# Performance work log

Measured on AMD Instinct MI355X. Metric: run time of the kernel, lower is better.

Reference implementation:

```python
import jax, jax.numpy as jnp
import numpy as np
import math

H = 128      # hidden_size
B = 4        # bsz
N = 32       # bsz * num_doc_per_q
L = 128      # doc_len


def setup_inputs() -> dict:
    key = jax.random.key(0)
    ks = jax.random.split(key, 7)
    word_ent_info = jax.random.normal(ks[0], (N, L, H), dtype=jnp.float32)
    word_ent_info_mask = jax.random.randint(ks[1], (N, L), 0, 2, dtype=jnp.int32)
    doc = jax.random.normal(ks[2], (N, L, H), dtype=jnp.float32)
    doc_mask = jax.random.randint(ks[3], (N, L), 0, 2, dtype=jnp.int32)
    q_for_text = jax.random.normal(ks[4], (B, H), dtype=jnp.float32)
    # nn.Linear(3H, H): weight [H, 3H], bias [H]
    W1 = jax.random.normal(ks[5], (H, 3 * H), dtype=jnp.float32) / math.sqrt(3 * H)
    b1 = jnp.zeros((H,), dtype=jnp.float32)
    # nn.Linear(H, 1): weight [1, H], bias [1]
    w2 = jax.random.normal(ks[6], (1, H), dtype=jnp.float32) / math.sqrt(H)
    b2 = jnp.zeros((1,), dtype=jnp.float32)
    return {"word_ent_info": word_ent_info, "word_ent_info_mask": word_ent_info_mask,
            "doc": doc, "doc_mask": doc_mask, "q_for_text": q_for_text,
            "W1": W1, "b1": b1, "w2": w2, "b2": b2}


def reference(word_ent_info, word_ent_info_mask, doc, doc_mask, q_for_text, W1, b1, w2, b2):
    n, l, h = doc.shape
    bsz = q_for_text.shape[0]
    dt = doc.dtype

    # word_ent_infoagg = mask^T @ word_ent_info -> [N, H]
    m = word_ent_info_mask.astype(dt)
    ent_agg = jnp.einsum('nl,nlh->nh', m, word_ent_info)

    # q expanded to one row per document: [N, H]
    q_exp = jnp.repeat(q_for_text, n // bsz, axis=0)

    # Split W1 over the concat([doc_self, ent_agg, q_agg]) feature axis.
    # score_pre[n,j,k,:] = W1a @ (doc_j*doc_k) + W1b @ (doc_j*ent_agg) + W1c @ (doc_k*q)
    W1a, W1b, W1c = jnp.split(W1, 3, axis=1)        # each [H, H]
    A = jnp.einsum('nje,nke,ge->njkg', doc, doc, W1a)          # [N,L,L,H]
    Bt = jnp.einsum('nje,ge->njg', doc * ent_agg[:, None, :], W1b)  # [N,L,H]
    Ct = jnp.einsum('nke,ge->nkg', doc * q_exp[:, None, :], W1c)    # [N,L,H]
    hid = jnp.tanh(A + Bt[:, :, None, :] + Ct[:, None, :, :] + b1)  # [N,L,L,H]

    score = (jnp.einsum('njkg,g->njk', hid, w2[0]) + b2[0]) / math.sqrt(h)

    dm = doc_mask.astype(dt)
    score_mask = dm[:, :, None] * dm[:, None, :]     # [N,L,L]
    score = jnp.where(score_mask == 0.0, jnp.asarray(-1e9, dt), score)
    w = jax.nn.softmax(score, axis=-1) * score_mask
    doc_ent_enc = jnp.einsum('njk,nkh->njh', w, doc)  # [N,L,H]
    return doc_ent_enc
```

## Files before the change

### kernel.cpp

```cpp
#include <hip/hip_runtime.h>
#include <hip/hip_bf16.h>
#include <math.h>

#define Hh 128
#define Nn 32
#define Ll 128
#define W1S 384
#define PAD 136

typedef __attribute__((ext_vector_type(8))) short short8;
typedef __attribute__((ext_vector_type(4))) float floatx4;

__device__ __forceinline__ unsigned short f2bf(float x) {
  __hip_bfloat16 h = __float2bfloat16(x);
  return __builtin_bit_cast(unsigned short, h);
}
__device__ __forceinline__ short8 pack8(float4 a, float4 b) {
  short8 r;
  r[0] = (short)f2bf(a.x); r[1] = (short)f2bf(a.y);
  r[2] = (short)f2bf(a.z); r[3] = (short)f2bf(a.w);
  r[4] = (short)f2bf(b.x); r[5] = (short)f2bf(b.y);
  r[6] = (short)f2bf(b.z); r[7] = (short)f2bf(b.w);
  return r;
}
__device__ __forceinline__ void mul4(float4& a, const float4& b) {
  a.x *= b.x; a.y *= b.y; a.z *= b.z; a.w *= b.w;
}

__launch_bounds__(256, 2)
__global__ void k_prep(const float* __restrict__ wei, const int* __restrict__ wmask,
                       const float* __restrict__ doc, const float* __restrict__ q,
                       const float* __restrict__ W1, const float* __restrict__ b1,
                       float* __restrict__ Bt, float* __restrict__ Ct,
                       short* __restrict__ W1ab) {
  __shared__ __align__(16) short Xs[Hh * PAD];
  __shared__ __align__(16) short Ws[Hh * PAD];
  __shared__ __align__(16) float red[2][Hh];
  __shared__ __align__(16) float ms[Hh];

  int bid = blockIdx.x;
  int n = bid >> 1, which = bid & 1;
  int tid = threadIdx.x;
  const float* docn = doc + (size_t)n * Ll * Hh;
  int e8 = (tid & 15) * 8, rsub = tid >> 4;

  if (which == 0) {
    int e = tid & 127, half = tid >> 7;
    const float* wp = wei + (size_t)n * Ll * Hh + (size_t)half * 64 * Hh + e;
    const int* mp = wmask + n * Ll + half * 64;
    float a = 0.f;
#pragma unroll 8
    for (int l = 0; l < 64; ++l) a = fmaf((float)mp[l], wp[(size_t)l * Hh], a);
    red[half][e] = a;
  } else {
    if (tid < Hh) ms[tid] = q[(size_t)(n >> 3) * Hh + tid];
  }
  if (tid < 32) {
    int row = which * 64 + n * 2 + (tid >> 4);
    int c8 = (tid & 15) * 8;
    const float4* wp = (const float4*)(W1 + (size_t)row * W1S + c8);
    *(short8*)(W1ab + row * Hh + c8) = pack8(wp[0], wp[1]);
  }
  const float* wbase = W1 + Hh + which * Hh;
#pragma unroll
  for (int p = 0; p < 8; ++p) {
    int row = p * 16 + rsub;
    const float4* wp = (const float4*)(wbase + (size_t)row * W1S + e8);
    *(short8*)(Ws + row * PAD + e8) = pack8(wp[0], wp[1]);
  }
  __syncthreads();
  if (which == 0 && tid < Hh) ms[tid] = red[0][tid] + red[1][tid];
  __syncthreads();

  {
    const float4* mp4 = (const float4*)(ms + e8);
    float4 m0 = mp4[0], m1 = mp4[1];
#pragma unroll
    for (int p = 0; p < 8; ++p) {
      int row = p * 16 + rsub;
      const float4* dp = (const float4*)(docn + (size_t)row * Hh + e8);
      float4 a = dp[0], b = dp[1];
      mul4(a, m0); mul4(b, m1);
      *(short8*)(Xs + row * PAD + e8) = pack8(a, b);
    }
  }
  __syncthreads();

  int lane = tid & 63, w = tid >> 6;
  int l15 = lane & 15, quad = lane >> 4;
  floatx4 acc[2][8];
#pragma unroll
  for (int mt = 0; mt < 2; ++mt)
#pragma unroll
    for (int nt = 0; nt < 8; ++nt) acc[mt][nt] = (floatx4){0.f, 0.f, 0.f, 0.f};
#pragma unroll
  for (int e0 = 0; e0 < Hh; e0 += 32) {
    int eo = e0 + quad * 8;
    short8 af[2], bfr[8];
    af[0] = *(const short8*)(Xs + (w * 32 + l15) * PAD + eo);
    af[1] = *(const short8*)(Xs + (w * 32 + 16 + l15) * PAD + eo);
#pragma unroll
    for (int nt = 0; nt < 8; ++nt)
      bfr[nt] = *(const short8*)(Ws + (nt * 16 + l15) * PAD + eo);
#pragma unroll
    for (int mt = 0; mt < 2; ++mt)
#pragma unroll
      for (int nt = 0; nt < 8; ++nt)
        acc[mt][nt] = __builtin_amdgcn_mfma_f32_16x16x32_bf16(af[mt], bfr[nt], acc[mt][nt], 0, 0, 0);
  }
  float* outp = (which ? Ct : Bt) + (size_t)n * Ll * Hh;
  float addv[8];
#pragma unroll
  for (int nt = 0; nt < 8; ++nt) addv[nt] = which ? 0.f : b1[nt * 16 + l15];
#pragma unroll
  for (int mt = 0; mt < 2; ++mt)
#pragma unroll
    for (int nt = 0; nt < 8; ++nt)
#pragma unroll
      for (int r = 0; r < 4; ++r) {
        int k = w * 32 + mt * 16 + quad * 4 + r;
        outp[(size_t)k * Hh + nt * 16 + l15] = acc[mt][nt][r] + addv[nt];
      }
}

__launch_bounds__(256, 2)
__global__ void k_main(const float* __restrict__ doc, const int* __restrict__ dmask,
                       const short* __restrict__ W1ab, const float* __restrict__ w2,
                       const float* __restrict__ b2,
                       const float* __restrict__ Bt, const float* __restrict__ Ct,
                       float* __restrict__ out) {
  __shared__ __align__(16) short Bg[Hh * PAD];
  __shared__ __align__(16) short Adj[Hh * PAD];
  __shared__ __align__(16) float sc[Ll];
  __shared__ __align__(16) float scwq[Ll][4];
  __shared__ __align__(16) float ored[2][4][Hh];

  int bid = blockIdx.x;
  int n = bid & 31, jq = bid >> 5;
  int tid = threadIdx.x;
  const float* docn = doc + (size_t)n * Ll * Hh;
  const int* dmn = dmask + n * Ll;
  int e8 = (tid & 15) * 8, rsub = tid >> 4;

#pragma unroll
  for (int p = 0; p < 8; ++p) {
    int row = p * 16 + rsub;
    *(short8*)(Bg + row * PAD + e8) = *(const short8*)(W1ab + row * Hh + e8);
  }

  int lane = tid & 63, w = tid >> 6;
  int l15 = lane & 15, quad = lane >> 4;
  const float c2 = 2.885390081777927f;
  const float inv = 0.088388347648318447f;
  float b2v = b2[0];
  float w2r[8];
#pragma unroll
  for (int nt = 0; nt < 8; ++nt) w2r[nt] = w2[nt * 16 + l15];
  const float* ctn = Ct + (size_t)n * Ll * Hh;
  int m0 = dmn[lane], m1 = dmn[lane + 64];

  for (int jv = 0; jv < 4; ++jv) {
    int j = jq * 4 + jv;
    if (dmn[j] == 0) {
      if (tid < Ll) scwq[tid][jv] = 0.f;
      continue;
    }
    {
      const float4* djp = (const float4*)(docn + (size_t)j * Hh + e8);
      float4 dj0 = djp[0], dj1 = djp[1];
#pragma unroll
      for (int p = 0; p < 8; ++p) {
        int row = p * 16 + rsub;
        const float4* dp = (const float4*)(docn + (size_t)row * Hh + e8);
        float4 a = dp[0], b = dp[1];
        mul4(a, dj0); mul4(b, dj1);
        *(short8*)(Adj + row * PAD + e8) = pack8(a, b);
      }
    }
    __syncthreads();

    floatx4 acc[2][8];
#pragma unroll
    for (int mt = 0; mt < 2; ++mt)
#pragma unroll
      for (int nt = 0; nt < 8; ++nt) acc[mt][nt] = (floatx4){0.f, 0.f, 0.f, 0.f};
#pragma unroll
    for (int e0 = 0; e0 < Hh; e0 += 32) {
      int eo = e0 + quad * 8;
      short8 af[2], bfr[8];
      af[0] = *(const short8*)(Adj + (w * 32 + l15) * PAD + eo);
      af[1] = *(const short8*)(Adj + (w * 32 + 16 + l15) * PAD + eo);
#pragma unroll
      for (int nt = 0; nt < 8; ++nt)
        bfr[nt] = *(const short8*)(Bg + (nt * 16 + l15) * PAD + eo);
#pragma unroll
      for (int mt = 0; mt < 2; ++mt)
#pragma unroll
        for (int nt = 0; nt < 8; ++nt)
          acc[mt][nt] = __builtin_amdgcn_mfma_f32_16x16x32_bf16(af[mt], bfr[nt], acc[mt][nt], 0, 0, 0);
    }

    const float* btrow = Bt + ((size_t)n * Ll + j) * Hh;
    float bbc[8];
#pragma unroll
    for (int nt = 0; nt < 8; ++nt) bbc[nt] = btrow[nt * 16 + l15] * c2;
#pragma unroll
    for (int mt = 0; mt < 2; ++mt) {
#pragma unroll
      for (int r = 0; r < 4; ++r) {
        int k = w * 32 + mt * 16 + quad * 4 + r;
        const float* ctp = ctn + (size_t)k * Hh + l15;
        float p = 0.f;
#pragma unroll
        for (int nt = 0; nt < 8; ++nt) {
          float s = acc[mt][nt][r] + ctp[nt * 16];
          float a2 = fmaf(s, c2, bbc[nt]);
          float e = exp2f(a2);
          float th = fmaf(-2.f, __builtin_amdgcn_rcpf(e + 1.f), 1.f);
          p = fmaf(th, w2r[nt], p);
        }
        p += __shfl_xor(p, 1);
        p += __shfl_xor(p, 2);
        p += __shfl_xor(p, 4);
        p += __shfl_xor(p, 8);
        if (l15 == 0) sc[k] = p;
      }
    }
    __syncthreads();

    {
      float s0 = m0 ? (sc[lane] + b2v) * inv : -1e9f;
      float s1 = m1 ? (sc[lane + 64] + b2v) * inv : -1e9f;
      float mx = fmaxf(s0, s1);
#pragma unroll
      for (int off = 32; off; off >>= 1) mx = fmaxf(mx, __shfl_xor(mx, off));
      float ex0 = __expf(s0 - mx), ex1 = __expf(s1 - mx);
      float sm = ex0 + ex1;
#pragma unroll
      for (int off = 32; off; off >>= 1) sm += __shfl_xor(sm, off);
      float rden = 1.f / sm;
      scwq[lane][jv] = m0 ? ex0 * rden : 0.f;
      scwq[lane + 64][jv] = m1 ? ex1 * rden : 0.f;
    }
  }
  __syncthreads();

  int half = tid >> 7, h = tid & 127;
  const float* dbase = docn + (size_t)half * 64 * Hh + h;
  float o0 = 0.f, o1 = 0.f, o2 = 0.f, o3 = 0.f;
#pragma unroll 8
  for (int kk = 0; kk < 64; ++kk) {
    float d = dbase[(size_t)kk * Hh];
    float4 wv = *(const float4*)&scwq[half * 64 + kk][0];
    o0 = fmaf(wv.x, d, o0); o1 = fmaf(wv.y, d, o1);
    o2 = fmaf(wv.z, d, o2); o3 = fmaf(wv.w, d, o3);
  }
  ored[half][0][h] = o0; ored[half][1][h] = o1;
  ored[half][2][h] = o2; ored[half][3][h] = o3;
  __syncthreads();
  if (tid < Ll) {
#pragma unroll
    for (int jv = 0; jv < 4; ++jv)
      out[((size_t)n * Ll + jq * 4 + jv) * Hh + tid] = ored[0][jv][tid] + ored[1][jv][tid];
  }
}

extern "C" void kernel_launch(void* const* d_in, const int* in_sizes, int n_in,
                              void* d_out, int out_size, void* d_ws, size_t ws_size,
                              hipStream_t stream) {
  const float* wei   = (const float*)d_in[0];
  const int*   wmask = (const int*)d_in[1];
  const float* doc   = (const float*)d_in[2];
  const int*   dmask = (const int*)d_in[3];
  const float* q     = (const float*)d_in[4];
  const float* W1    = (const float*)d_in[5];
  const float* b1    = (const float*)d_in[6];
  const float* w2    = (const float*)d_in[7];
  const float* b2    = (const float*)d_in[8];
  float* out = (float*)d_out;

  float* ws   = (float*)d_ws;
  float* Bt   = ws;
  float* Ct   = Bt + (size_t)Nn * Ll * Hh;
  short* W1ab = (short*)(Ct + (size_t)Nn * Ll * Hh);

  k_prep<<<2 * Nn, 256, 0, stream>>>(wei, wmask, doc, q, W1, b1, Bt, Ct, W1ab);
  k_main<<<Nn * Ll / 4, 256, 0, stream>>>(doc, dmask, W1ab, w2, b2, Bt, Ct, out);
}
```

Measured before the change: 137.9 us.

## Build doc_j*doc_k operand in registers from bf16 doc and store Ct in bf16

k_prep now writes a bf16 copy of doc and stores Ct as bf16, and k_main converts W1a to bf16 itself. k_main keeps each wave's doc_k rows in registers as bf16 fragments and forms the doc_j*doc_k MFMA A operand in registers per j. This drops the per-j LDS staging of the Adj tile and its barrier, and halves the Ct read traffic. LDS per block shrinks and launch bounds rise to 3 blocks per CU. The product is now formed from bf16-rounded inputs and Ct is rounded to bf16, which adds some numerical error.

```diff
diff --git a/kernel.cpp b/kernel.cpp
--- a/kernel.cpp
+++ b/kernel.cpp
@@ -14,6 +14,10 @@
 __device__ __forceinline__ unsigned short f2bf(float x) {
   __hip_bfloat16 h = __float2bfloat16(x);
   return __builtin_bit_cast(unsigned short, h);
+}
+__device__ __forceinline__ float bf2f(short s) {
+  unsigned int u = ((unsigned int)(unsigned short)s) << 16;
+  return __builtin_bit_cast(float, u);
 }
 __device__ __forceinline__ short8 pack8(float4 a, float4 b) {
   short8 r;
@@ -31,8 +35,8 @@
 __global__ void k_prep(const float* __restrict__ wei, const int* __restrict__ wmask,
                        const float* __restrict__ doc, const float* __restrict__ q,
                        const float* __restrict__ W1, const float* __restrict__ b1,
-                       float* __restrict__ Bt, float* __restrict__ Ct,
-                       short* __restrict__ W1ab) {
+                       float* __restrict__ Bt, unsigned short* __restrict__ Ctb,
+                       short* __restrict__ docb) {
   __shared__ __align__(16) short Xs[Hh * PAD];
   __shared__ __align__(16) short Ws[Hh * PAD];
   __shared__ __align__(16) float red[2][Hh];
@@ -55,11 +59,14 @@
   } else {
     if (tid < Hh) ms[tid] = q[(size_t)(n >> 3) * Hh + tid];
   }
-  if (tid < 32) {
-    int row = which * 64 + n * 2 + (tid >> 4);
-    int c8 = (tid & 15) * 8;
-    const float4* wp = (const float4*)(W1 + (size_t)row * W1S + c8);
-    *(short8*)(W1ab + row * Hh + c8) = pack8(wp[0], wp[1]);
+  {
+    int row = which * 64 + (tid >> 2);
+    int c32 = (tid & 3) * 32;
+    const float4* dp = (const float4*)(docn + (size_t)row * Hh + c32);
+    short* ob = docb + ((size_t)n * Ll + row) * Hh + c32;
+#pragma unroll
+    for (int i = 0; i < 4; ++i)
+      *(short8*)(ob + i * 8) = pack8(dp[2 * i], dp[2 * i + 1]);
   }
   const float* wbase = W1 + Hh + which * Hh;
 #pragma unroll
@@ -108,30 +115,42 @@
       for (int nt = 0; nt < 8; ++nt)
         acc[mt][nt] = __builtin_amdgcn_mfma_f32_16x16x32_bf16(af[mt], bfr[nt], acc[mt][nt], 0, 0, 0);
   }
-  float* outp = (which ? Ct : Bt) + (size_t)n * Ll * Hh;
-  float addv[8];
-#pragma unroll
-  for (int nt = 0; nt < 8; ++nt) addv[nt] = which ? 0.f : b1[nt * 16 + l15];
-#pragma unroll
-  for (int mt = 0; mt < 2; ++mt)
-#pragma unroll
-    for (int nt = 0; nt < 8; ++nt)
-#pragma unroll
-      for (int r = 0; r < 4; ++r) {
-        int k = w * 32 + mt * 16 + quad * 4 + r;
-        outp[(size_t)k * Hh + nt * 16 + l15] = acc[mt][nt][r] + addv[nt];
-      }
-}
-
-__launch_bounds__(256, 2)
+  if (which == 0) {
+    float* outp = Bt + (size_t)n * Ll * Hh;
+    float addv[8];
+#pragma unroll
+    for (int nt = 0; nt < 8; ++nt) addv[nt] = b1[nt * 16 + l15];
+#pragma unroll
+    for (int mt = 0; mt < 2; ++mt)
+#pragma unroll
+      for (int nt = 0; nt < 8; ++nt)
+#pragma unroll
+        for (int r = 0; r < 4; ++r) {
+          int k = w * 32 + mt * 16 + quad * 4 + r;
+          outp[(size_t)k * Hh + nt * 16 + l15] = acc[mt][nt][r] + addv[nt];
+        }
+  } else {
+    unsigned short* outp = Ctb + (size_t)n * Ll * Hh;
+#pragma unroll
+    for (int mt = 0; mt < 2; ++mt)
+#pragma unroll
+      for (int nt = 0; nt < 8; ++nt)
+#pragma unroll
+        for (int r = 0; r < 4; ++r) {
+          int k = w * 32 + mt * 16 + quad * 4 + r;
+          outp[(size_t)k * Hh + nt * 16 + l15] = f2bf(acc[mt][nt][r]);
+        }
+  }
+}
+
+__launch_bounds__(256, 3)
 __global__ void k_main(const float* __restrict__ doc, const int* __restrict__ dmask,
-                       const short* __restrict__ W1ab, const float* __restrict__ w2,
+                       const float* __restrict__ W1, const float* __restrict__ w2,
                        const float* __restrict__ b2,
-                       const float* __restrict__ Bt, const float* __restrict__ Ct,
-                       float* __restrict__ out) {
-  __shared__ __align__(16) short Bg[Hh * PAD];
-  __shared__ __align__(16) short Adj[Hh * PAD];
-  __shared__ __align__(16) float sc[Ll];
+                       const float* __restrict__ Bt, const unsigned short* __restrict__ Ctb,
+                       const short* __restrict__ docb, float* __restrict__ out) {
+  __shared__ __align__(16) short Wa[Hh * PAD];
+  __shared__ __align__(16) float sc[4][Ll];
   __shared__ __align__(16) float scwq[Ll][4];
   __shared__ __align__(16) float ored[2][4][Hh];
 
@@ -139,25 +158,36 @@
   int n = bid & 31, jq = bid >> 5;
   int tid = threadIdx.x;
   const float* docn = doc + (size_t)n * Ll * Hh;
+  const short* dbn = docb + (size_t)n * Ll * Hh;
   const int* dmn = dmask + n * Ll;
   int e8 = (tid & 15) * 8, rsub = tid >> 4;
 
 #pragma unroll
   for (int p = 0; p < 8; ++p) {
     int row = p * 16 + rsub;
-    *(short8*)(Bg + row * PAD + e8) = *(const short8*)(W1ab + row * Hh + e8);
+    const float4* wp = (const float4*)(W1 + (size_t)row * W1S + e8);
+    *(short8*)(Wa + row * PAD + e8) = pack8(wp[0], wp[1]);
   }
 
   int lane = tid & 63, w = tid >> 6;
   int l15 = lane & 15, quad = lane >> 4;
+
+  short8 afr[2][4];
+#pragma unroll
+  for (int mt = 0; mt < 2; ++mt)
+#pragma unroll
+    for (int c = 0; c < 4; ++c)
+      afr[mt][c] = *(const short8*)(dbn + (size_t)(w * 32 + mt * 16 + l15) * Hh + c * 32 + quad * 8);
+
+  float w2r[8];
+#pragma unroll
+  for (int nt = 0; nt < 8; ++nt) w2r[nt] = w2[nt * 16 + l15];
+  int m0 = dmn[lane], m1 = dmn[lane + 64];
+  float b2v = b2[0];
   const float c2 = 2.885390081777927f;
   const float inv = 0.088388347648318447f;
-  float b2v = b2[0];
-  float w2r[8];
-#pragma unroll
-  for (int nt = 0; nt < 8; ++nt) w2r[nt] = w2[nt * 16 + l15];
-  const float* ctn = Ct + (size_t)n * Ll * Hh;
-  int m0 = dmn[lane], m1 = dmn[lane + 64];
+  const unsigned short* ctn = Ctb + (size_t)n * Ll * Hh;
+  __syncthreads();
 
   for (int jv = 0; jv < 4; ++jv) {
     int j = jq * 4 + jv;
@@ -165,39 +195,36 @@
       if (tid < Ll) scwq[tid][jv] = 0.f;
       continue;
     }
-    {
-      const float4* djp = (const float4*)(docn + (size_t)j * Hh + e8);
-      float4 dj0 = djp[0], dj1 = djp[1];
-#pragma unroll
-      for (int p = 0; p < 8; ++p) {
-        int row = p * 16 + rsub;
-        const float4* dp = (const float4*)(docn + (size_t)row * Hh + e8);
-        float4 a = dp[0], b = dp[1];
-        mul4(a, dj0); mul4(b, dj1);
-        *(short8*)(Adj + row * PAD + e8) = pack8(a, b);
+    floatx4 acc[2][8];
+#pragma unroll
+    for (int mt = 0; mt < 2; ++mt)
+#pragma unroll
+      for (int nt = 0; nt < 8; ++nt) acc[mt][nt] = (floatx4){0.f, 0.f, 0.f, 0.f};
+
+#pragma unroll
+    for (int c = 0; c < 4; ++c) {
+      int eo = c * 32 + quad * 8;
+      short8 djs = *(const short8*)(dbn + (size_t)j * Hh + eo);
+      float djf[8];
+#pragma unroll
+      for (int i = 0; i < 8; ++i) djf[i] = bf2f(djs[i]);
+      short8 afs[2];
+#pragma unroll
+      for (int mt = 0; mt < 2; ++mt) {
+        short8 r;
+#pragma unroll
+        for (int i = 0; i < 8; ++i) r[i] = (short)f2bf(bf2f(afr[mt][c][i]) * djf[i]);
+        afs[mt] = r;
       }
-    }
-    __syncthreads();
-
-    floatx4 acc[2][8];
-#pragma unroll
-    for (int mt = 0; mt < 2; ++mt)
-#pragma unroll
-      for (int nt = 0; nt < 8; ++nt) acc[mt][nt] = (floatx4){0.f, 0.f, 0.f, 0.f};
-#pragma unroll
-    for (int e0 = 0; e0 < Hh; e0 += 32) {
-      int eo = e0 + quad * 8;
-      short8 af[2], bfr[8];
-      af[0] = *(const short8*)(Adj + (w * 32 + l15) * PAD + eo);
-      af[1] = *(const short8*)(Adj + (w * 32 + 16 + l15) * PAD + eo);
+      short8 bfr[8];
 #pragma unroll
       for (int nt = 0; nt < 8; ++nt)
-        bfr[nt] = *(const short8*)(Bg + (nt * 16 + l15) * PAD + eo);
+        bfr[nt] = *(const short8*)(Wa + (nt * 16 + l15) * PAD + eo);
 #pragma unroll
       for (int mt = 0; mt < 2; ++mt)
 #pragma unroll
         for (int nt = 0; nt < 8; ++nt)
-          acc[mt][nt] = __builtin_amdgcn_mfma_f32_16x16x32_bf16(af[mt], bfr[nt], acc[mt][nt], 0, 0, 0);
+          acc[mt][nt] = __builtin_amdgcn_mfma_f32_16x16x32_bf16(afs[mt], bfr[nt], acc[mt][nt], 0, 0, 0);
     }
 
     const float* btrow = Bt + ((size_t)n * Ll + j) * Hh;
@@ -209,11 +236,11 @@
 #pragma unroll
       for (int r = 0; r < 4; ++r) {
         int k = w * 32 + mt * 16 + quad * 4 + r;
-        const float* ctp = ctn + (size_t)k * Hh + l15;
+        const unsigned short* ctp = ctn + (size_t)k * Hh + l15;
         float p = 0.f;
 #pragma unroll
         for (int nt = 0; nt < 8; ++nt) {
-          float s = acc[mt][nt][r] + ctp[nt * 16];
+          float s = acc[mt][nt][r] + bf2f((short)ctp[nt * 16]);
           float a2 = fmaf(s, c2, bbc[nt]);
           float e = exp2f(a2);
           float th = fmaf(-2.f, __builtin_amdgcn_rcpf(e + 1.f), 1.f);
@@ -223,14 +250,14 @@
         p += __shfl_xor(p, 2);
         p += __shfl_xor(p, 4);
         p += __shfl_xor(p, 8);
-        if (l15 == 0) sc[k] = p;
+        if (l15 == 0) sc[jv][k] = p;
       }
     }
     __syncthreads();
 
     {
-      float s0 = m0 ? (sc[lane] + b2v) * inv : -1e9f;
-      float s1 = m1 ? (sc[lane + 64] + b2v) * inv : -1e9f;
+      float s0 = m0 ? (sc[jv][lane] + b2v) * inv : -1e9f;
+      float s1 = m1 ? (sc[jv][lane + 64] + b2v) * inv : -1e9f;
       float mx = fmaxf(s0, s1);
 #pragma unroll
       for (int off = 32; off; off >>= 1) mx = fmaxf(mx, __shfl_xor(mx, off));
@@ -279,11 +306,11 @@
   const float* b2    = (const float*)d_in[8];
   float* out = (float*)d_out;
 
-  float* ws   = (float*)d_ws;
-  float* Bt   = ws;
-  float* Ct   = Bt + (size_t)Nn * Ll * Hh;
-  short* W1ab = (short*)(Ct + (size_t)Nn * Ll * Hh);
-
-  k_prep<<<2 * Nn, 256, 0, stream>>>(wei, wmask, doc, q, W1, b1, Bt, Ct, W1ab);
-  k_main<<<Nn * Ll / 4, 256, 0, stream>>>(doc, dmask, W1ab, w2, b2, Bt, Ct, out);
-}
+  float* ws = (float*)d_ws;
+  float*          Bt   = ws;
+  unsigned short* Ctb  = (unsigned short*)(Bt + (size_t)Nn * Ll * Hh);
+  short*          docb = (short*)(Ctb + (size_t)Nn * Ll * Hh);
+
+  k_prep<<<2 * Nn, 256, 0, stream>>>(wei, wmask, doc, q, W1, b1, Bt, Ctb, docb);
+  k_main<<<Nn * Ll / 4, 256, 0, stream>>>(doc, dmask, W1, w2, b2, Bt, Ctb, docb, out);
+}
```

New measurement: 181.1 us. 31.3% more time.
